# Kernel optimization log

Hardware: AMD Instinct MI355X
Metric: run time of the kernel (lower is better)

The kernel has to match this reference:

```python
import jax, jax.numpy as jnp
import numpy as np

B, S, D_IN, H, HEADS, CF = 16384, 64, 4, 32, 2, 16
DH = H // HEADS  # per-head dim = 16


def setup_inputs() -> dict:
    key = jax.random.key(0)
    ks = jax.random.split(key, 32)
    def w(k, shape, scale=0.1):
        return jax.random.normal(k, shape, dtype=jnp.float32) * scale
    return {
        "x": jax.random.normal(ks[0], (B, S, D_IN), dtype=jnp.float32),
        # ConvBranch
        "c1w": w(ks[1], (CF, D_IN, 3)), "c1b": w(ks[2], (CF,)),
        "c2w": w(ks[3], (CF, CF, 3)),  "c2b": w(ks[4], (CF,)),
        "cpw": w(ks[5], (H, CF)),      "cpb": w(ks[6], (H,)),
        # AttentionBranch
        "ipw": w(ks[7], (H, D_IN)),    "ipb": w(ks[8], (H,)),
        "wq": w(ks[9], (H, H)),  "bq": w(ks[10], (H,)),
        "wk": w(ks[11], (H, H)), "bk": w(ks[12], (H,)),
        "wv": w(ks[13], (H, H)), "bv": w(ks[14], (H,)),
        "wo": w(ks[15], (H, H)), "bo": w(ks[16], (H,)),
        "lng": jnp.ones((H,), jnp.float32), "lnb": jnp.zeros((H,), jnp.float32),
        # DBMM
        "gw": w(ks[17], (2 * H, 2 * H)), "gb": w(ks[18], (2 * H,)),
        "pw": w(ks[19], (H, 2 * H)),     "pb": w(ks[20], (H,)),
        # Output head
        "h1w": w(ks[21], (16, H)), "h1b": w(ks[22], (16,)),
        "h2w": w(ks[23], (2, 16)), "h2b": w(ks[24], (2,)),
    }


def _forward(x, c1w, c1b, c2w, c2b, cpw, cpb, ipw, ipb,
             wq, bq, wk, bk, wv, bv, wo, bo, lng, lnb,
             gw, gb, pw, pb, h1w, h1b, h2w, h2b):
    # ---- ConvBranch: (B,S,4) -> (B,32) ----
    xt = jnp.transpose(x, (0, 2, 1))  # (B, C=4, S)
    dn = ("NCH", "OIH", "NCH")
    h1 = jax.nn.relu(jax.lax.conv_general_dilated(xt, c1w, (1,), [(1, 1)], dimension_numbers=dn) + c1b[None, :, None])
    h2 = jax.nn.relu(jax.lax.conv_general_dilated(h1, c2w, (1,), [(1, 1)], dimension_numbers=dn) + c2b[None, :, None])
    pooled = jnp.mean(h2, axis=-1)               # (B, CF) AdaptiveAvgPool1d(1)
    conv_feat = pooled @ cpw.T + cpb             # (B, 32)

    # ---- AttentionBranch: (B,S,4) -> (B,32) ----
    h = x @ ipw.T + ipb                          # (B, S, 32)
    q = (h @ wq.T + bq).reshape(B, S, HEADS, DH)
    k = (h @ wk.T + bk).reshape(B, S, HEADS, DH)
    v = (h @ wv.T + bv).reshape(B, S, HEADS, DH)
    scores = jnp.einsum("bqhd,bkhd->bhqk", q, k) / jnp.sqrt(jnp.float32(DH))
    attn = jax.nn.softmax(scores, axis=-1)       # dropout=eval no-op
    ctx = jnp.einsum("bhqk,bkhd->bqhd", attn, v).reshape(B, S, H)
    attn_out = ctx @ wo.T + bo
    y = h + attn_out
    mu = jnp.mean(y, axis=-1, keepdims=True)
    var = jnp.var(y, axis=-1, keepdims=True)
    y = (y - mu) / jnp.sqrt(var + 1e-5) * lng + lnb
    att_feat = jnp.mean(y, axis=1)               # (B, 32)

    # ---- DBMM fusion ----
    combined = jnp.concatenate([conv_feat, att_feat], axis=-1)  # (B, 64)
    gated = combined * jax.nn.sigmoid(combined @ gw.T + gb)
    fused = gated @ pw.T + pb                    # (B, 32); dropout eval no-op

    # ---- Output head ----
    out = jax.nn.relu(fused @ h1w.T + h1b) @ h2w.T + h2b        # (B, 2)
    return out


def reference(x, c1w, c1b, c2w, c2b, cpw, cpb, ipw, ipb,
              wq, bq, wk, bk, wv, bv, wo, bo, lng, lnb,
              gw, gb, pw, pb, h1w, h1b, h2w, h2b):
    return _forward(x, c1w, c1b, c2w, c2b, cpw, cpb, ipw, ipb,
                    wq, bq, wk, bk, wv, bv, wo, bo, lng, lnb,
                    gw, gb, pw, pb, h1w, h1b, h2w, h2b)
```

## Files before the change

### kernel.cpp

```cpp
#include <hip/hip_runtime.h>
#include <math.h>

#define S 64
#define DIN 4
#define H 32
#define CF 16
#define DH 16
#define WPB 4

typedef __attribute__((ext_vector_type(8))) short bf16x8;
typedef __attribute__((ext_vector_type(4))) short s16x4;
typedef __attribute__((ext_vector_type(4))) float f32x4;

#define MFMA(a, b, c) __builtin_amdgcn_mfma_f32_16x16x32_bf16((a), (b), (c), 0, 0, 0)

__device__ __forceinline__ void wsync() {
    asm volatile("" ::: "memory");
    __builtin_amdgcn_wave_barrier();
    asm volatile("" ::: "memory");
}

__device__ __forceinline__ short f2bf(float f) {
    union { float f; unsigned u; } v; v.f = f;
    unsigned r = (v.u + 0x7FFFu + ((v.u >> 16) & 1u)) >> 16;
    return (short)r;
}

__device__ __forceinline__ bf16x8 frag8(const float* p) {
    f32x4 a = *(const f32x4*)p;
    f32x4 b = *(const f32x4*)(p + 4);
    bf16x8 f;
    f[0] = f2bf(a[0]); f[1] = f2bf(a[1]); f[2] = f2bf(a[2]); f[3] = f2bf(a[3]);
    f[4] = f2bf(b[0]); f[5] = f2bf(b[1]); f[6] = f2bf(b[2]); f[7] = f2bf(b[3]);
    return f;
}

__device__ __forceinline__ s16x4 pack4(float a, float b, float c, float d) {
    s16x4 v; v[0] = f2bf(a); v[1] = f2bf(b); v[2] = f2bf(c); v[3] = f2bf(d); return v;
}


__global__ __launch_bounds__(WPB * 64, 2)
void fused_fwd(const float* __restrict__ x,
               const float* __restrict__ c1w, const float* __restrict__ c1b,
               const float* __restrict__ c2w, const float* __restrict__ c2b,
               const float* __restrict__ cpw, const float* __restrict__ cpb,
               const float* __restrict__ ipw, const float* __restrict__ ipb,
               const float* __restrict__ wq, const float* __restrict__ bq,
               const float* __restrict__ wk, const float* __restrict__ bk,
               const float* __restrict__ wv, const float* __restrict__ bv,
               const float* __restrict__ wo, const float* __restrict__ bo,
               const float* __restrict__ lng, const float* __restrict__ lnb,
               const float* __restrict__ gw, const float* __restrict__ gb,
               const float* __restrict__ pw, const float* __restrict__ pb,
               const float* __restrict__ h1w, const float* __restrict__ h1b,
               const float* __restrict__ h2w, const float* __restrict__ h2b,
               float* __restrict__ out)
{
    __shared__ __attribute__((aligned(16))) float hA_all[WPB * S * 36];
    __shared__ __attribute__((aligned(16))) short R_all[WPB * S * 48];
    __shared__ __attribute__((aligned(16))) short Vt_all[WPB * 16 * 72];
    __shared__ __attribute__((aligned(16))) float smc_all[WPB * 192];

    const int w  = threadIdx.x >> 6;
    const int s  = threadIdx.x & 63;
    const int fr = s & 15;
    const int g  = s >> 4;
    const int b  = blockIdx.x * WPB + w;

    float* hA  = hA_all  + w * (S * 36);
    short* R   = R_all   + w * (S * 48);
    short* Vt  = Vt_all  + w * (16 * 72);
    float* smc = smc_all + w * 192;

    const f32x4 xr = reinterpret_cast<const f32x4*>(x)[b * S + s];
    float x0[4] = {xr[0], xr[1], xr[2], xr[3]};

    float xm[4], xp[4];
#pragma unroll
    for (int i = 0; i < 4; ++i) {
        float up = __shfl_up(x0[i], 1);
        float dn = __shfl_down(x0[i], 1);
        xm[i] = (s > 0) ? up : 0.f;
        xp[i] = (s < S - 1) ? dn : 0.f;
    }
    float hc[CF];
#pragma unroll
    for (int o = 0; o < CF; ++o) {
        float acc = c1b[o];
#pragma unroll
        for (int i = 0; i < DIN; ++i) {
            acc += xm[i] * c1w[(o * DIN + i) * 3 + 0];
            acc += x0[i] * c1w[(o * DIN + i) * 3 + 1];
            acc += xp[i] * c1w[(o * DIN + i) * 3 + 2];
        }
        hc[o] = fmaxf(acc, 0.f);
    }
    float hm[CF], hp[CF];
#pragma unroll
    for (int o = 0; o < CF; ++o) {
        float up = __shfl_up(hc[o], 1);
        float dn = __shfl_down(hc[o], 1);
        hm[o] = (s > 0) ? up : 0.f;
        hp[o] = (s < S - 1) ? dn : 0.f;
    }
    float h2r[CF];
#pragma unroll
    for (int o = 0; o < CF; ++o) {
        float acc = c2b[o];
#pragma unroll
        for (int i = 0; i < CF; ++i) {
            acc += hm[i] * c2w[(o * CF + i) * 3 + 0];
            acc += hc[i] * c2w[(o * CF + i) * 3 + 1];
            acc += hp[i] * c2w[(o * CF + i) * 3 + 2];
        }
        h2r[o] = fmaxf(acc, 0.f);
    }
#pragma unroll
    for (int o = 0; o < CF; ++o) {
        float v = h2r[o];
#pragma unroll
        for (int off = 32; off > 0; off >>= 1) v += __shfl_xor(v, off);
        h2r[o] = v * (1.f / 64.f);
    }
    if (s < H) {
        float acc = cpb[s];
#pragma unroll
        for (int o = 0; o < CF; ++o) acc += h2r[o] * cpw[s * CF + o];
        smc[s] = acc;
    }

    {
        float hr[H];
#pragma unroll
        for (int j = 0; j < H; ++j) {
            hr[j] = ipb[j] + x0[0] * ipw[j * 4 + 0] + x0[1] * ipw[j * 4 + 1]
                           + x0[2] * ipw[j * 4 + 2] + x0[3] * ipw[j * 4 + 3];
        }
#pragma unroll
        for (int i = 0; i < 8; ++i) {
            f32x4 t = {hr[4 * i], hr[4 * i + 1], hr[4 * i + 2], hr[4 * i + 3]};
            *(f32x4*)&hA[s * 36 + 4 * i] = t;
        }
    }
    wsync();

    const bf16x8 z8 = {0, 0, 0, 0, 0, 0, 0, 0};
    const f32x4  z4 = {0.f, 0.f, 0.f, 0.f};

    f32x4 yD[2][4];
#pragma unroll
    for (int mt = 0; mt < 2; ++mt) {
        f32x4 bo4 = *(const f32x4*)&bo[mt * 16 + g * 4];
#pragma unroll
        for (int nt = 0; nt < 4; ++nt) yD[mt][nt] = bo4;
    }

#pragma unroll
    for (int h = 0; h < 2; ++h) {
        bf16x8 hF[4];
#pragma unroll
        for (int t = 0; t < 4; ++t) hF[t] = frag8(&hA[(t * 16 + fr) * 36 + g * 8]);

        bf16x8 wqF = frag8(&wq[(h * 16 + fr) * 32 + g * 8]);
        bf16x8 wkF = frag8(&wk[(h * 16 + fr) * 32 + g * 8]);
        bf16x8 wvF = frag8(&wv[(h * 16 + fr) * 32 + g * 8]);
        f32x4 bq4 = *(const f32x4*)&bq[h * 16 + g * 4];
        f32x4 bk4 = *(const f32x4*)&bk[h * 16 + g * 4];
        float bvv = bv[h * 16 + fr];

#pragma unroll
        for (int nt = 0; nt < 4; ++nt) {
            f32x4 aq = MFMA(wqF, hF[nt], bq4);
            *(s16x4*)&R[(nt * 16 + fr) * 48 + g * 4] =
                pack4(aq[0] * 0.25f, aq[1] * 0.25f, aq[2] * 0.25f, aq[3] * 0.25f);
            f32x4 ak = MFMA(wkF, hF[nt], bk4);
            *(s16x4*)&R[(nt * 16 + fr) * 48 + 16 + g * 4] =
                pack4(ak[0], ak[1], ak[2], ak[3]);
        }
#pragma unroll
        for (int mi = 0; mi < 4; ++mi) {
            f32x4 cv = {bvv, bvv, bvv, bvv};
            f32x4 av = MFMA(hF[mi], wvF, cv);
            *(s16x4*)&Vt[fr * 72 + mi * 16 + g * 4] = pack4(av[0], av[1], av[2], av[3]);
        }
        wsync();

        bf16x8 qF[4], kF[4];
#pragma unroll
        for (int t = 0; t < 4; ++t) {
            bf16x8 fq = z8, fk = z8;
            if (g < 2) {
                fq = *(const bf16x8*)&R[(t * 16 + fr) * 48 + g * 8];
                fk = *(const bf16x8*)&R[(t * 16 + fr) * 48 + 16 + g * 8];
            }
            qF[t] = fq; kF[t] = fk;
        }
        f32x4 pA[4][4];
#pragma unroll
        for (int mi = 0; mi < 4; ++mi)
#pragma unroll
            for (int nj = 0; nj < 4; ++nj)
                pA[mi][nj] = MFMA(kF[mi], qF[nj], z4);

        float inv[4];
#pragma unroll
        for (int nj = 0; nj < 4; ++nj) {
            float l = 0.f;
#pragma unroll
            for (int mi = 0; mi < 4; ++mi)
#pragma unroll
                for (int r = 0; r < 4; ++r) {
                    float e = __expf(pA[mi][nj][r]);
                    pA[mi][nj][r] = e;
                    l += e;
                }
            l += __shfl_xor(l, 16);
            l += __shfl_xor(l, 32);
            inv[nj] = 1.0f / l;
        }

        f32x4 cAcc[4] = {z4, z4, z4, z4};
#pragma unroll
        for (int kk = 0; kk < 2; ++kk) {
            wsync();
#pragma unroll
            for (int m2 = 0; m2 < 2; ++m2) {
                const int mi = kk * 2 + m2;
#pragma unroll
                for (int nj = 0; nj < 4; ++nj)
                    *(s16x4*)&R[(nj * 16 + fr) * 40 + m2 * 16 + g * 4] =
                        pack4(pA[mi][nj][0] * inv[nj], pA[mi][nj][1] * inv[nj],
                              pA[mi][nj][2] * inv[nj], pA[mi][nj][3] * inv[nj]);
            }
            wsync();
            bf16x8 vtF = *(const bf16x8*)&Vt[fr * 72 + kk * 32 + g * 8];
#pragma unroll
            for (int nt = 0; nt < 4; ++nt) {
                bf16x8 ptF = *(const bf16x8*)&R[(nt * 16 + fr) * 40 + g * 8];
                cAcc[nt] = MFMA(vtF, ptF, cAcc[nt]);
            }
        }
        wsync();

#pragma unroll
        for (int nt = 0; nt < 4; ++nt)
            *(s16x4*)&R[(nt * 16 + fr) * 40 + g * 4] =
                pack4(cAcc[nt][0], cAcc[nt][1], cAcc[nt][2], cAcc[nt][3]);
        wsync();

        bf16x8 woF[2];
#pragma unroll
        for (int mt = 0; mt < 2; ++mt) {
            bf16x8 f = frag8(&wo[(mt * 16 + fr) * 32 + h * 16 + (g & 1) * 8]);
            if (g >= 2) f = z8;
            woF[mt] = f;
        }
#pragma unroll
        for (int nt = 0; nt < 4; ++nt) {
            bf16x8 cF = *(const bf16x8*)&R[(nt * 16 + fr) * 40 + g * 8];
#pragma unroll
            for (int mt = 0; mt < 2; ++mt)
                yD[mt][nt] = MFMA(woF[mt], cF, yD[mt][nt]);
        }
        wsync();
    }

#pragma unroll
    for (int mt = 0; mt < 2; ++mt)
#pragma unroll
        for (int nt = 0; nt < 4; ++nt) {
            f32x4 hh = *(const f32x4*)&hA[(nt * 16 + fr) * 36 + mt * 16 + g * 4];
#pragma unroll
            for (int r = 0; r < 4; ++r) yD[mt][nt][r] += hh[r];
        }
    f32x4 lg0 = *(const f32x4*)&lng[g * 4];
    f32x4 lg1 = *(const f32x4*)&lng[16 + g * 4];
    f32x4 lb0 = *(const f32x4*)&lnb[g * 4];
    f32x4 lb1 = *(const f32x4*)&lnb[16 + g * 4];
#pragma unroll
    for (int nt = 0; nt < 4; ++nt) {
        float sy = 0.f, sy2 = 0.f;
#pragma unroll
        for (int mt = 0; mt < 2; ++mt)
#pragma unroll
            for (int r = 0; r < 4; ++r) {
                float v = yD[mt][nt][r];
                sy += v; sy2 += v * v;
            }
        sy  += __shfl_xor(sy, 16);  sy  += __shfl_xor(sy, 32);
        sy2 += __shfl_xor(sy2, 16); sy2 += __shfl_xor(sy2, 32);
        const float mu   = sy * (1.f / 32.f);
        const float var  = sy2 * (1.f / 32.f) - mu * mu;
        const float rstd = rsqrtf(var + 1e-5f);
#pragma unroll
        for (int r = 0; r < 4; ++r) {
            yD[0][nt][r] = (yD[0][nt][r] - mu) * rstd * lg0[r] + lb0[r];
            yD[1][nt][r] = (yD[1][nt][r] - mu) * rstd * lg1[r] + lb1[r];
        }
    }

#pragma unroll
    for (int mt = 0; mt < 2; ++mt)
#pragma unroll
        for (int r = 0; r < 4; ++r) {
            float af = yD[mt][0][r] + yD[mt][1][r] + yD[mt][2][r] + yD[mt][3][r];
            af += __shfl_xor(af, 1);
            af += __shfl_xor(af, 2);
            af += __shfl_xor(af, 4);
            af += __shfl_xor(af, 8);
            if (fr == 0) smc[H + mt * 16 + g * 4 + r] = af * (1.f / 64.f);
        }
    wsync();

    {
        const int j = s;
        float acc = gb[j];
        const f32x4* smc4 = (const f32x4*)smc;
        const f32x4* gw4  = (const f32x4*)&gw[j * 2 * H];
#pragma unroll
        for (int k4 = 0; k4 < 16; ++k4) {
            f32x4 cv = smc4[k4], wv4 = gw4[k4];
            acc += cv[0] * wv4[0] + cv[1] * wv4[1] + cv[2] * wv4[2] + cv[3] * wv4[3];
        }
        const float sig = 1.f / (1.f + __expf(-acc));
        smc[64 + j] = smc[j] * sig;
    }
    wsync();
    if (s < H) {
        float acc = pb[s];
        const f32x4* smc4 = (const f32x4*)(smc + 64);
        const f32x4* pw4  = (const f32x4*)&pw[s * 2 * H];
#pragma unroll
        for (int k4 = 0; k4 < 16; ++k4) {
            f32x4 cv = smc4[k4], wv4 = pw4[k4];
            acc += cv[0] * wv4[0] + cv[1] * wv4[1] + cv[2] * wv4[2] + cv[3] * wv4[3];
        }
        smc[128 + s] = acc;
    }
    wsync();
    if (s < 16) {
        float acc = h1b[s];
#pragma unroll
        for (int c = 0; c < H; ++c) acc += smc[128 + c] * h1w[s * H + c];
        smc[160 + s] = fmaxf(acc, 0.f);
    }
    wsync();
    if (s < 2) {
        float acc = h2b[s];
#pragma unroll
        for (int c = 0; c < 16; ++c) acc += smc[160 + c] * h2w[s * 16 + c];
        out[b * 2 + s] = acc;
    }
}

extern "C" void kernel_launch(void* const* d_in, const int* in_sizes, int n_in,
                              void* d_out, int out_size, void* d_ws, size_t ws_size,
                              hipStream_t stream) {
    (void)n_in; (void)d_ws; (void)ws_size; (void)in_sizes;
    const int nb = out_size / 2;
    const float* xp_ = (const float*)d_in[0];
    const float* c1w = (const float*)d_in[1];  const float* c1b = (const float*)d_in[2];
    const float* c2w = (const float*)d_in[3];  const float* c2b = (const float*)d_in[4];
    const float* cpw = (const float*)d_in[5];  const float* cpb = (const float*)d_in[6];
    const float* ipw = (const float*)d_in[7];  const float* ipb = (const float*)d_in[8];
    const float* wq  = (const float*)d_in[9];  const float* bq  = (const float*)d_in[10];
    const float* wk  = (const float*)d_in[11]; const float* bk  = (const float*)d_in[12];
    const float* wv  = (const float*)d_in[13]; const float* bv  = (const float*)d_in[14];
    const float* wo  = (const float*)d_in[15]; const float* bo  = (const float*)d_in[16];
    const float* lng = (const float*)d_in[17]; const float* lnb = (const float*)d_in[18];
    const float* gw  = (const float*)d_in[19]; const float* gb  = (const float*)d_in[20];
    const float* pw  = (const float*)d_in[21]; const float* pb  = (const float*)d_in[22];
    const float* h1w = (const float*)d_in[23]; const float* h1b = (const float*)d_in[24];
    const float* h2w = (const float*)d_in[25]; const float* h2b = (const float*)d_in[26];
    float* outp = (float*)d_out;

    dim3 grid(nb / WPB), block(WPB * 64);
    hipLaunchKernelGGL(fused_fwd, grid, block, 0, stream,
                       xp_, c1w, c1b, c2w, c2b, cpw, cpb, ipw, ipb,
                       wq, bq, wk, bk, wv, bv, wo, bo, lng, lnb,
                       gw, gb, pw, pb, h1w, h1b, h2w, h2b, outp);
}
```

Before: 298.1 us.

## Shrink LDS footprint: bf16 hidden buffer, recompute residual, defer softmax normalization

Result: faster. 248.7 us (-16.6%).

```diff
diff --git a/kernel.cpp b/kernel.cpp
--- a/kernel.cpp
+++ b/kernel.cpp
@@ -1,11 +1,11 @@
 #include <hip/hip_runtime.h>
+#include <hip/hip_bf16.h>
 #include <math.h>
 
 #define S 64
 #define DIN 4
 #define H 32
 #define CF 16
-#define DH 16
 #define WPB 4
 
 typedef __attribute__((ext_vector_type(8))) short bf16x8;
@@ -21,9 +21,8 @@
 }
 
 __device__ __forceinline__ short f2bf(float f) {
-    union { float f; unsigned u; } v; v.f = f;
-    unsigned r = (v.u + 0x7FFFu + ((v.u >> 16) & 1u)) >> 16;
-    return (short)r;
+    __hip_bfloat16 h = __float2bfloat16(f);
+    return *reinterpret_cast<short*>(&h);
 }
 
 __device__ __forceinline__ bf16x8 frag8(const float* p) {
@@ -57,10 +56,8 @@
                const float* __restrict__ h2w, const float* __restrict__ h2b,
                float* __restrict__ out)
 {
-    __shared__ __attribute__((aligned(16))) float hA_all[WPB * S * 36];
-    __shared__ __attribute__((aligned(16))) short R_all[WPB * S * 48];
-    __shared__ __attribute__((aligned(16))) short Vt_all[WPB * 16 * 72];
-    __shared__ __attribute__((aligned(16))) float smc_all[WPB * 192];
+    __shared__ __attribute__((aligned(16))) short R_all[WPB * 2560];
+    __shared__ __attribute__((aligned(16))) short U_all[WPB * 2560];
 
     const int w  = threadIdx.x >> 6;
     const int s  = threadIdx.x & 63;
@@ -68,10 +65,11 @@
     const int g  = s >> 4;
     const int b  = blockIdx.x * WPB + w;
 
-    float* hA  = hA_all  + w * (S * 36);
-    short* R   = R_all   + w * (S * 48);
-    short* Vt  = Vt_all  + w * (16 * 72);
-    float* smc = smc_all + w * 192;
+    short* R   = R_all + w * 2560;
+    short* U   = U_all + w * 2560;
+    short* hB  = U;
+    short* Vt  = U;
+    float* smc = reinterpret_cast<float*>(U + 1152);
 
     const f32x4 xr = reinterpret_cast<const f32x4*>(x)[b * S + s];
     float x0[4] = {xr[0], xr[1], xr[2], xr[3]};
@@ -123,11 +121,12 @@
         for (int off = 32; off > 0; off >>= 1) v += __shfl_xor(v, off);
         h2r[o] = v * (1.f / 64.f);
     }
+    float convf = 0.f;
     if (s < H) {
         float acc = cpb[s];
 #pragma unroll
         for (int o = 0; o < CF; ++o) acc += h2r[o] * cpw[s * CF + o];
-        smc[s] = acc;
+        convf = acc;
     }
 
     {
@@ -138,11 +137,19 @@
                            + x0[2] * ipw[j * 4 + 2] + x0[3] * ipw[j * 4 + 3];
         }
 #pragma unroll
-        for (int i = 0; i < 8; ++i) {
-            f32x4 t = {hr[4 * i], hr[4 * i + 1], hr[4 * i + 2], hr[4 * i + 3]};
-            *(f32x4*)&hA[s * 36 + 4 * i] = t;
-        }
-    }
+        for (int i = 0; i < 4; ++i) {
+            bf16x8 t;
+#pragma unroll
+            for (int e = 0; e < 8; ++e) t[e] = f2bf(hr[i * 8 + e]);
+            *(bf16x8*)&hB[s * 40 + i * 8] = t;
+        }
+    }
+    wsync();
+
+    bf16x8 hF[4];
+#pragma unroll
+    for (int t = 0; t < 4; ++t) hF[t] = *(const bf16x8*)&hB[(t * 16 + fr) * 40 + g * 8];
+    if (s < H) smc[s] = convf;
     wsync();
 
     const bf16x8 z8 = {0, 0, 0, 0, 0, 0, 0, 0};
@@ -158,10 +165,6 @@
 
 #pragma unroll
     for (int h = 0; h < 2; ++h) {
-        bf16x8 hF[4];
-#pragma unroll
-        for (int t = 0; t < 4; ++t) hF[t] = frag8(&hA[(t * 16 + fr) * 36 + g * 8]);
-
         bf16x8 wqF = frag8(&wq[(h * 16 + fr) * 32 + g * 8]);
         bf16x8 wkF = frag8(&wk[(h * 16 + fr) * 32 + g * 8]);
         bf16x8 wvF = frag8(&wv[(h * 16 + fr) * 32 + g * 8]);
@@ -172,10 +175,10 @@
 #pragma unroll
         for (int nt = 0; nt < 4; ++nt) {
             f32x4 aq = MFMA(wqF, hF[nt], bq4);
-            *(s16x4*)&R[(nt * 16 + fr) * 48 + g * 4] =
+            *(s16x4*)&R[(nt * 16 + fr) * 40 + g * 4] =
                 pack4(aq[0] * 0.25f, aq[1] * 0.25f, aq[2] * 0.25f, aq[3] * 0.25f);
             f32x4 ak = MFMA(wkF, hF[nt], bk4);
-            *(s16x4*)&R[(nt * 16 + fr) * 48 + 16 + g * 4] =
+            *(s16x4*)&R[(nt * 16 + fr) * 40 + 24 + g * 4] =
                 pack4(ak[0], ak[1], ak[2], ak[3]);
         }
 #pragma unroll
@@ -191,8 +194,8 @@
         for (int t = 0; t < 4; ++t) {
             bf16x8 fq = z8, fk = z8;
             if (g < 2) {
-                fq = *(const bf16x8*)&R[(t * 16 + fr) * 48 + g * 8];
-                fk = *(const bf16x8*)&R[(t * 16 + fr) * 48 + 16 + g * 8];
+                fq = *(const bf16x8*)&R[(t * 16 + fr) * 40 + g * 8];
+                fk = *(const bf16x8*)&R[(t * 16 + fr) * 40 + 24 + g * 8];
             }
             qF[t] = fq; kF[t] = fk;
         }
@@ -230,8 +233,8 @@
 #pragma unroll
                 for (int nj = 0; nj < 4; ++nj)
                     *(s16x4*)&R[(nj * 16 + fr) * 40 + m2 * 16 + g * 4] =
-                        pack4(pA[mi][nj][0] * inv[nj], pA[mi][nj][1] * inv[nj],
-                              pA[mi][nj][2] * inv[nj], pA[mi][nj][3] * inv[nj]);
+                        pack4(pA[mi][nj][0], pA[mi][nj][1],
+                              pA[mi][nj][2], pA[mi][nj][3]);
             }
             wsync();
             bf16x8 vtF = *(const bf16x8*)&Vt[fr * 72 + kk * 32 + g * 8];
@@ -241,6 +244,10 @@
                 cAcc[nt] = MFMA(vtF, ptF, cAcc[nt]);
             }
         }
+#pragma unroll
+        for (int nt = 0; nt < 4; ++nt)
+#pragma unroll
+            for (int r = 0; r < 4; ++r) cAcc[nt][r] *= inv[nt];
         wsync();
 
 #pragma unroll
@@ -258,7 +265,8 @@
         }
 #pragma unroll
         for (int nt = 0; nt < 4; ++nt) {
-            bf16x8 cF = *(const bf16x8*)&R[(nt * 16 + fr) * 40 + g * 8];
+            bf16x8 cF = z8;
+            if (g < 2) cF = *(const bf16x8*)&R[(nt * 16 + fr) * 40 + g * 8];
 #pragma unroll
             for (int mt = 0; mt < 2; ++mt)
                 yD[mt][nt] = MFMA(woF[mt], cF, yD[mt][nt]);
@@ -266,14 +274,24 @@
         wsync();
     }
 
-#pragma unroll
-    for (int mt = 0; mt < 2; ++mt)
-#pragma unroll
-        for (int nt = 0; nt < 4; ++nt) {
-            f32x4 hh = *(const f32x4*)&hA[(nt * 16 + fr) * 36 + mt * 16 + g * 4];
-#pragma unroll
-            for (int r = 0; r < 4; ++r) yD[mt][nt][r] += hh[r];
-        }
+    {
+        f32x4 xq[4];
+#pragma unroll
+        for (int nt = 0; nt < 4; ++nt)
+            xq[nt] = reinterpret_cast<const f32x4*>(x)[b * S + nt * 16 + fr];
+#pragma unroll
+        for (int mt = 0; mt < 2; ++mt)
+#pragma unroll
+            for (int r = 0; r < 4; ++r) {
+                const int j = mt * 16 + g * 4 + r;
+                const f32x4 wr4 = *(const f32x4*)&ipw[j * 4];
+                const float bb = ipb[j];
+#pragma unroll
+                for (int nt = 0; nt < 4; ++nt)
+                    yD[mt][nt][r] += bb + xq[nt][0] * wr4[0] + xq[nt][1] * wr4[1]
+                                        + xq[nt][2] * wr4[2] + xq[nt][3] * wr4[3];
+            }
+    }
     f32x4 lg0 = *(const f32x4*)&lng[g * 4];
     f32x4 lg1 = *(const f32x4*)&lng[16 + g * 4];
     f32x4 lb0 = *(const f32x4*)&lnb[g * 4];
```
